# Kernel optimization log

Measured on AMD Instinct MI355X. Metric: run time of the kernel, lower is better.

The kernel has to match this reference:

```python
import jax, jax.numpy as jnp
import numpy as np

EPS = 1e-10
LOSS_COEF = 0.01

def cv_squared(v):
    # torch .var() is unbiased (ddof=1)
    return jnp.var(v, ddof=1) / (jnp.mean(v) ** 2 + EPS)

def setup_inputs() -> dict:
    B, Q, D, H, O, E = 4096, 256, 512, 1024, 512, 16
    key = jax.random.key(0)
    ks = jax.random.split(key, 8)
    return {
        "query": jax.random.normal(ks[0], (B, Q), jnp.float32),
        "x": jax.random.normal(ks[1], (B, D), jnp.float32),
        "w_gate": jax.random.normal(ks[2], (D, E), jnp.float32) * 0.02,
        "task_gate": jax.random.normal(ks[3], (Q, E), jnp.float32) * 0.02,
        "W1": jax.random.normal(ks[4], (E, D, H), jnp.float32) * 0.02,
        "b1": jnp.zeros((E, H), jnp.float32),
        "W2": jax.random.normal(ks[5], (E, H, O), jnp.float32) * 0.02,
        "b2": jnp.zeros((E, O), jnp.float32),
        "k": 4,
    }

def reference(query, x, w_gate, task_gate, W1, b1, W2, b2, k):
    B = x.shape[0]
    E = w_gate.shape[1]
    # --- top-k gating (eval mode: clean logits, no noise) ---
    logits = x @ w_gate + query @ task_gate                      # [B, E]
    m = min(k + 1, E)
    top_vals, top_idx = jax.lax.top_k(logits, m)                 # [B, m]
    topk_gates = jax.nn.softmax(top_vals[:, :k], axis=1)         # [B, k]
    rows = jnp.arange(B)[:, None]
    gates = jnp.zeros_like(logits).at[rows, top_idx[:, :k]].set(topk_gates)  # [B, E]
    importance = gates.sum(0)                                    # [E]
    load = (gates > 0).sum(0).astype(jnp.float32)                # [E]
    loss = LOSS_COEF * (cv_squared(importance) + cv_squared(load))
    # --- dispatch / expert MLP / combine ---
    # gate==0 contributions vanish, so weighting by gates is exactly
    # equivalent to the sparse gather -> expert -> index_add combine.
    y = jnp.zeros((B, W2.shape[2]), jnp.float32)
    for e in range(E):  # fixed small loop over experts
        h = jax.nn.relu(x @ W1[e] + b1[e])                       # [B, H]
        out = h @ W2[e] + b2[e]                                  # [B, O]
        y = y + gates[:, e:e + 1] * out
    return y, loss
```

## Files before the change

kernel.cpp:

```cpp
#include <hip/hip_runtime.h>

typedef short bf16x8_t __attribute__((ext_vector_type(8)));
typedef short bf16x4_t __attribute__((ext_vector_type(4)));
typedef float f32x4_t __attribute__((ext_vector_type(4)));

#define B_DIM 4096
#define Q_DIM 256
#define D_DIM 512
#define H_DIM 1024
#define O_DIM 512
#define E_NUM 16
#define K_TOP 4

#define BM 128
#define BN 128
#define BK 32

__device__ __forceinline__ short f2bf(float f) {
  unsigned int u = __float_as_uint(f);
  u += 0x7FFFu + ((u >> 16) & 1u);
  return (short)(u >> 16);
}

__device__ __forceinline__ void g2l16(const void* g, void* l) {
  __builtin_amdgcn_global_load_lds(
      (const __attribute__((address_space(1))) void*)(unsigned long long)(size_t)g,
      (__attribute__((address_space(3))) void*)(unsigned)(size_t)l, 16, 0, 0);
}

__device__ __forceinline__ void tr_tile(float (*tile)[65], const float* __restrict__ s,
                                        short* __restrict__ d, int R, int C, int r0, int c0,
                                        int t) {
#pragma unroll
  for (int i = 0; i < 16; i++) {
    int lin = i * 256 + t;
    int rr = lin >> 6, cc = lin & 63;
    tile[rr][cc] = s[(size_t)(r0 + rr) * C + (c0 + cc)];
  }
  __syncthreads();
#pragma unroll
  for (int i = 0; i < 2; i++) {
    int task = i * 256 + t;
    int cr = task >> 3, g = task & 7;
    bf16x8_t v;
#pragma unroll
    for (int j = 0; j < 8; j++) v[j] = f2bf(tile[g * 8 + j][cr]);
    *(bf16x8_t*)(d + (size_t)(c0 + cr) * R + r0 + g * 8) = v;
  }
}

__global__ __launch_bounds__(256) void weights_prep(
    const float* __restrict__ W1, const float* __restrict__ W2,
    const float* __restrict__ wg, const float* __restrict__ tg,
    short* __restrict__ w1t, short* __restrict__ w2t, float* __restrict__ wpack) {
  __shared__ float tile[64][65];
  const int blk = blockIdx.x, t = threadIdx.x;
  if (blk < 2048) {
    int e = blk >> 7, rem = blk & 127;
    int r0 = (rem >> 4) * 64, c0 = (rem & 15) * 64;
    tr_tile(tile, W1 + (size_t)e * D_DIM * H_DIM, w1t + (size_t)e * D_DIM * H_DIM,
            D_DIM, H_DIM, r0, c0, t);
  } else if (blk < 4096) {
    int b2 = blk - 2048;
    int e = b2 >> 7, rem = b2 & 127;
    int r0 = (rem >> 3) * 64, c0 = (rem & 7) * 64;
    tr_tile(tile, W2 + (size_t)e * H_DIM * O_DIM, w2t + (size_t)e * H_DIM * O_DIM,
            H_DIM, O_DIM, r0, c0, t);
  } else {
    int lin = (blk - 4096) * 256 + t;
    if (lin < E_NUM * 768) {
      int e = lin / 768, r = lin % 768;
      wpack[lin] = (r < D_DIM) ? wg[r * E_NUM + e] : tg[(r - D_DIM) * E_NUM + e];
    }
  }
}

__global__ __launch_bounds__(256) void gating_kernel(
    const float* __restrict__ x, const float* __restrict__ query,
    const float* __restrict__ wpack,
    int4* __restrict__ topk_e4, float4* __restrict__ topk_g4, short* __restrict__ x_bf) {
  __shared__ __align__(16) float4 s_w[E_NUM * 192];
  const int t = threadIdx.x, wv = t >> 6, lane = t & 63;
  const float4* wp4 = (const float4*)wpack;
#pragma unroll
  for (int i = 0; i < 12; i++) s_w[i * 256 + t] = wp4[i * 256 + t];
  __syncthreads();

  const int row = blockIdx.x * 4 + wv;
  const float4* xr = (const float4*)(x + (size_t)row * D_DIM);
  const float4* qr = (const float4*)(query + (size_t)row * Q_DIM);
  const float4 xv0 = xr[lane], xv1 = xr[64 + lane], qv = qr[lane];

  {
    bf16x4_t v0, v1;
    v0[0] = f2bf(xv0.x); v0[1] = f2bf(xv0.y); v0[2] = f2bf(xv0.z); v0[3] = f2bf(xv0.w);
    v1[0] = f2bf(xv1.x); v1[1] = f2bf(xv1.y); v1[2] = f2bf(xv1.z); v1[3] = f2bf(xv1.w);
    short* xb = x_bf + (size_t)row * D_DIM;
    *(bf16x4_t*)(xb + lane * 4) = v0;
    *(bf16x4_t*)(xb + 256 + lane * 4) = v1;
  }

  float p[E_NUM];
#pragma unroll
  for (int e = 0; e < E_NUM; e++) {
    float4 w0 = s_w[e * 192 + lane];
    float4 w1 = s_w[e * 192 + 64 + lane];
    float4 wq = s_w[e * 192 + 128 + lane];
    p[e] = xv0.x * w0.x + xv0.y * w0.y + xv0.z * w0.z + xv0.w * w0.w +
           xv1.x * w1.x + xv1.y * w1.y + xv1.z * w1.z + xv1.w * w1.w +
           qv.x * wq.x + qv.y * wq.y + qv.z * wq.z + qv.w * wq.w;
  }
#pragma unroll
  for (int e = 0; e < E_NUM; e++) {
    p[e] += __shfl_xor(p[e], 16, 64);
    p[e] += __shfl_xor(p[e], 32, 64);
  }
#pragma unroll
  for (int s = 8; s >= 1; s >>= 1) {
    const bool take = (lane & s) != 0;
#pragma unroll
    for (int j = 0; j < s; j++) {
      float keep = take ? p[j + s] : p[j];
      float send = take ? p[j] : p[j + s];
      p[j] = keep + __shfl_xor(send, s, 64);
    }
  }
  const float logit = p[0];
  float v[E_NUM];
#pragma unroll
  for (int i = 0; i < E_NUM; i++) v[i] = __shfl(logit, i, 64);

  if (lane == 0) {
    int idx[K_TOP];
    float val[K_TOP];
    unsigned used = 0;
    for (int k = 0; k < K_TOP; k++) {
      float best = -3.4e38f;
      int bi = 0;
      for (int i = 0; i < E_NUM; i++)
        if (!(used & (1u << i)) && v[i] > best) { best = v[i]; bi = i; }
      used |= 1u << bi;
      idx[k] = bi;
      val[k] = best;
    }
    float mx = val[0];
    float ex[K_TOP], Z = 0.f;
    for (int k = 0; k < K_TOP; k++) { ex[k] = __expf(val[k] - mx); Z += ex[k]; }
    topk_e4[row] = make_int4(idx[0], idx[1], idx[2], idx[3]);
    topk_g4[row] = make_float4(ex[0] / Z, ex[1] / Z, ex[2] / Z, ex[3] / Z);
  }
}

__global__ __launch_bounds__(256) void csr_kernel(
    const int4* __restrict__ topk_e4, const float4* __restrict__ topk_g4,
    int* __restrict__ count, float* __restrict__ imp_g,
    int* __restrict__ rowlist, int* __restrict__ slotid, float* __restrict__ egate) {
  const int e = blockIdx.x, t = threadIdx.x;
  __shared__ int s_cnt[256];
  __shared__ float s_gs[64];
  int c = 0;
  float gs = 0.f;
#pragma unroll 4
  for (int i = 0; i < 16; i++) {
    int row = t * 16 + i;
    int4 v = topk_e4[row];
    float4 g = topk_g4[row];
    if (v.x == e) { c++; gs += g.x; }
    if (v.y == e) { c++; gs += g.y; }
    if (v.z == e) { c++; gs += g.z; }
    if (v.w == e) { c++; gs += g.w; }
  }
  s_cnt[t] = c;
  float gw = gs;
  for (int off = 32; off >= 1; off >>= 1) gw += __shfl_down(gw, off, 64);
  if ((t & 63) == 0) s_gs[t >> 6] = gw;
  __syncthreads();
  for (int off = 1; off < 256; off <<= 1) {
    int vv = (t >= off) ? s_cnt[t - off] : 0;
    __syncthreads();
    s_cnt[t] += vv;
    __syncthreads();
  }
  int pos = s_cnt[t] - c;
#pragma unroll 4
  for (int i = 0; i < 16; i++) {
    int row = t * 16 + i;
    int4 v = topk_e4[row];
    float4 g = topk_g4[row];
    int ve[4] = {v.x, v.y, v.z, v.w};
    float vg[4] = {g.x, g.y, g.z, g.w};
#pragma unroll
    for (int k = 0; k < K_TOP; k++) {
      if (ve[k] == e) {
        rowlist[e * B_DIM + pos] = row;
        slotid[e * B_DIM + pos] = row * K_TOP + k;
        egate[e * B_DIM + pos] = vg[k];
        pos++;
      }
    }
  }
  if (t == 0) {
    count[e] = s_cnt[255];
    imp_g[e] = s_gs[0] + s_gs[1] + s_gs[2] + s_gs[3];
  }
}

__global__ __launch_bounds__(64) void loss_offsets_kernel(
    const int* __restrict__ count, const float* __restrict__ imp_g,
    int* __restrict__ offs, float* __restrict__ out_loss) {
  if (threadIdx.x == 0) {
    float mi = 0.f, ml = 0.f;
    for (int i = 0; i < E_NUM; i++) { mi += imp_g[i]; ml += (float)count[i]; }
    mi /= (float)E_NUM;
    ml /= (float)E_NUM;
    float vi = 0.f, vl = 0.f;
    for (int i = 0; i < E_NUM; i++) {
      float di = imp_g[i] - mi;
      vi += di * di;
      float dl = (float)count[i] - ml;
      vl += dl * dl;
    }
    vi /= (float)(E_NUM - 1);
    vl /= (float)(E_NUM - 1);
    out_loss[0] = 0.01f * (vi / (mi * mi + 1e-10f) + vl / (ml * ml + 1e-10f));
    int run = 0;
    for (int i = 0; i < E_NUM; i++) { offs[i] = run; run += count[i]; }
  }
}

__global__ __launch_bounds__(256) void gemm1_kernel(
    const short* __restrict__ x_bf, const short* __restrict__ w1t,
    const float* __restrict__ b1, const int* __restrict__ count,
    const int* __restrict__ offs, const int* __restrict__ rowlist,
    short* __restrict__ h_buf) {
  const int flat = blockIdx.x;
  const int xcd = flat & 7, j = flat >> 3;
  const int mt = j & 31, gidx = j >> 5;
  const int group = xcd * 16 + gidx;
  const int e = group >> 3, nt = group & 7;
  const int n_e = count[e];
  if (mt * BM >= n_e) return;
  __shared__ __align__(16) short As[BM * BK];
  __shared__ __align__(16) short Bs[BN * BK];
  const int t = threadIdx.x, lane = t & 63, wv = t >> 6;
  const int wm = wv >> 1, wn = wv & 1;
  const int srow = wv * 16 + (lane >> 2);
  const int kb = (lane & 3) * 8;
  int gr0 = mt * BM + srow;       gr0 = gr0 < n_e ? gr0 : n_e - 1;
  int gr1 = mt * BM + 64 + srow;  gr1 = gr1 < n_e ? gr1 : n_e - 1;
  const short* pa0 = x_bf + (size_t)rowlist[e * B_DIM + gr0] * D_DIM + kb;
  const short* pa1 = x_bf + (size_t)rowlist[e * B_DIM + gr1] * D_DIM + kb;
  const short* w1te = w1t + ((size_t)e * H_DIM + nt * BN) * D_DIM;
  const short* pb0 = w1te + (size_t)srow * D_DIM + kb;
  const short* pb1 = w1te + (size_t)(64 + srow) * D_DIM + kb;
  short* lA0 = As + wv * 16 * BK;
  short* lA1 = As + (64 + wv * 16) * BK;
  short* lB0 = Bs + wv * 16 * BK;
  short* lB1 = Bs + (64 + wv * 16) * BK;

  f32x4_t acc[4][4] = {};
  const int frow = lane & 15, kg = lane >> 4;

  for (int k0 = 0; k0 < D_DIM; k0 += BK) {
    g2l16(pa0 + k0, lA0);
    g2l16(pa1 + k0, lA1);
    g2l16(pb0 + k0, lB0);
    g2l16(pb1 + k0, lB1);
    __syncthreads();
    bf16x8_t af[4], bfr[4];
#pragma unroll
    for (int mi = 0; mi < 4; mi++)
      af[mi] = *(const bf16x8_t*)&As[(wm * 64 + mi * 16 + frow) * BK + kg * 8];
#pragma unroll
    for (int ni = 0; ni < 4; ni++)
      bfr[ni] = *(const bf16x8_t*)&Bs[(wn * 64 + ni * 16 + frow) * BK + kg * 8];
#pragma unroll
    for (int mi = 0; mi < 4; mi++)
#pragma unroll
      for (int ni = 0; ni < 4; ni++)
        acc[mi][ni] = __builtin_amdgcn_mfma_f32_16x16x32_bf16(af[mi], bfr[ni], acc[mi][ni], 0, 0, 0);
    __syncthreads();
  }
  const int obase = offs[e];
#pragma unroll
  for (int mi = 0; mi < 4; mi++) {
#pragma unroll
    for (int r = 0; r < 4; r++) {
      int row = wm * 64 + mi * 16 + kg * 4 + r;
      int m_local = mt * BM + row;
      if (m_local >= n_e) continue;
      size_t hrow = (size_t)(obase + m_local) * H_DIM;
#pragma unroll
      for (int ni = 0; ni < 4; ni++) {
        int col = nt * BN + wn * 64 + ni * 16 + frow;
        float vv = acc[mi][ni][r] + b1[e * H_DIM + col];
        h_buf[hrow + col] = f2bf(vv > 0.f ? vv : 0.f);
      }
    }
  }
}

__global__ __launch_bounds__(256) void gemm2_kernel(
    const short* __restrict__ h_buf, const short* __restrict__ w2t,
    const float* __restrict__ b2, const int* __restrict__ count,
    const int* __restrict__ offs, const int* __restrict__ slotid,
    const float* __restrict__ egate, float* __restrict__ out_buf) {
  const int flat = blockIdx.x;
  const int xcd = flat & 7, j = flat >> 3;
  const int nt = j & 3, gidx = j >> 2;
  const int group = xcd * 64 + gidx;
  const int e = group >> 5, mt = group & 31;
  const int n_e = count[e];
  if (mt * BM >= n_e) return;
  __shared__ __align__(16) short As[BM * BK];
  __shared__ __align__(16) short Bs[BN * BK];
  const int t = threadIdx.x, lane = t & 63, wv = t >> 6;
  const int wm = wv >> 1, wn = wv & 1;
  const int srow = wv * 16 + (lane >> 2);
  const int kb = (lane & 3) * 8;
  const int obase = offs[e];
  int gr0 = mt * BM + srow;       gr0 = gr0 < n_e ? gr0 : n_e - 1;
  int gr1 = mt * BM + 64 + srow;  gr1 = gr1 < n_e ? gr1 : n_e - 1;
  const short* pa0 = h_buf + (size_t)(obase + gr0) * H_DIM + kb;
  const short* pa1 = h_buf + (size_t)(obase + gr1) * H_DIM + kb;
  const short* w2te = w2t + ((size_t)e * O_DIM + nt * BN) * H_DIM;
  const short* pb0 = w2te + (size_t)srow * H_DIM + kb;
  const short* pb1 = w2te + (size_t)(64 + srow) * H_DIM + kb;
  short* lA0 = As + wv * 16 * BK;
  short* lA1 = As + (64 + wv * 16) * BK;
  short* lB0 = Bs + wv * 16 * BK;
  short* lB1 = Bs + (64 + wv * 16) * BK;

  f32x4_t acc[4][4] = {};
  const int frow = lane & 15, kg = lane >> 4;

  for (int k0 = 0; k0 < H_DIM; k0 += BK) {
    g2l16(pa0 + k0, lA0);
    g2l16(pa1 + k0, lA1);
    g2l16(pb0 + k0, lB0);
    g2l16(pb1 + k0, lB1);
    __syncthreads();
    bf16x8_t af[4], bfr[4];
#pragma unroll
    for (int mi = 0; mi < 4; mi++)
      af[mi] = *(const bf16x8_t*)&As[(wm * 64 + mi * 16 + frow) * BK + kg * 8];
#pragma unroll
    for (int ni = 0; ni < 4; ni++)
      bfr[ni] = *(const bf16x8_t*)&Bs[(wn * 64 + ni * 16 + frow) * BK + kg * 8];
#pragma unroll
    for (int mi = 0; mi < 4; mi++)
#pragma unroll
      for (int ni = 0; ni < 4; ni++)
        acc[mi][ni] = __builtin_amdgcn_mfma_f32_16x16x32_bf16(af[mi], bfr[ni], acc[mi][ni], 0, 0, 0);
    __syncthreads();
  }
#pragma unroll
  for (int mi = 0; mi < 4; mi++) {
#pragma unroll
    for (int r = 0; r < 4; r++) {
      int row = wm * 64 + mi * 16 + kg * 4 + r;
      int m_local = mt * BM + row;
      if (m_local >= n_e) continue;
      float g = egate[e * B_DIM + m_local];
      size_t orow = (size_t)slotid[e * B_DIM + m_local] * O_DIM;
#pragma unroll
      for (int ni = 0; ni < 4; ni++) {
        int col = nt * BN + wn * 64 + ni * 16 + frow;
        out_buf[orow + col] = (acc[mi][ni][r] + b2[e * O_DIM + col]) * g;
      }
    }
  }
}

__global__ __launch_bounds__(256) void combine_kernel(const float* __restrict__ out_buf,
                                                      float* __restrict__ y) {
  int idx = blockIdx.x * 256 + threadIdx.x;
  int b = idx >> 7;
  int o = (idx & 127) << 2;
  const float* base = out_buf + (size_t)b * K_TOP * O_DIM + o;
  float4 a0 = *(const float4*)(base);
  float4 a1 = *(const float4*)(base + O_DIM);
  float4 a2 = *(const float4*)(base + 2 * O_DIM);
  float4 a3 = *(const float4*)(base + 3 * O_DIM);
  float4 r;
  r.x = a0.x + a1.x + a2.x + a3.x;
  r.y = a0.y + a1.y + a2.y + a3.y;
  r.z = a0.z + a1.z + a2.z + a3.z;
  r.w = a0.w + a1.w + a2.w + a3.w;
  *(float4*)(y + (size_t)b * O_DIM + o) = r;
}

extern "C" void kernel_launch(void* const* d_in, const int* in_sizes, int n_in,
                              void* d_out, int out_size, void* d_ws, size_t ws_size,
                              hipStream_t stream) {
  (void)in_sizes; (void)n_in; (void)out_size; (void)ws_size;
  const float* query = (const float*)d_in[0];
  const float* x = (const float*)d_in[1];
  const float* wg = (const float*)d_in[2];
  const float* tg = (const float*)d_in[3];
  const float* W1 = (const float*)d_in[4];
  const float* b1 = (const float*)d_in[5];
  const float* W2 = (const float*)d_in[6];
  const float* b2 = (const float*)d_in[7];
  float* y = (float*)d_out;

  char* ws = (char*)d_ws;
  int* count = (int*)(ws + 0);
  float* imp = (float*)(ws + 64);
  int* offs = (int*)(ws + 128);
  int* rowlist = (int*)(ws + 256);
  int* slotid = (int*)(ws + 262400);
  float* egate = (float*)(ws + 524544);
  int4* topk_e4 = (int4*)(ws + 786688);
  float4* topk_g4 = (float4*)(ws + 852224);
  float* wpack = (float*)(ws + 917760);
  short* h_buf = (short*)(ws + 1048576);
  short* w2t = (short*)(ws + 34603008);
  short* x_bf = (short*)(ws + 51380224);
  short* w1t = (short*)(ws + 55574528);
  float* out_buf = (float*)(ws + 51380224);

  weights_prep<<<dim3(4144), 256, 0, stream>>>(W1, W2, wg, tg, w1t, w2t, wpack);
  gating_kernel<<<dim3(B_DIM / 4), 256, 0, stream>>>(x, query, wpack, topk_e4, topk_g4, x_bf);
  csr_kernel<<<dim3(E_NUM), 256, 0, stream>>>(topk_e4, topk_g4, count, imp,
                                              rowlist, slotid, egate);
  loss_offsets_kernel<<<1, 64, 0, stream>>>(count, imp, offs, y + (size_t)B_DIM * O_DIM);
  gemm1_kernel<<<dim3(4096), 256, 0, stream>>>(x_bf, w1t, b1, count, offs, rowlist, h_buf);
  gemm2_kernel<<<dim3(2048), 256, 0, stream>>>(h_buf, w2t, b2, count, offs, slotid, egate,
                                               out_buf);
  combine_kernel<<<dim3(B_DIM * O_DIM / 4 / 256), 256, 0, stream>>>(out_buf, y);
}
```

Baseline: 235.8 us.

## Fuse weight prep with gating and fold loss/offsets into CSR kernel

```diff
diff --git a/kernel.cpp b/kernel.cpp
--- a/kernel.cpp
+++ b/kernel.cpp
@@ -49,44 +49,57 @@
   }
 }
 
-__global__ __launch_bounds__(256) void weights_prep(
+__global__ __launch_bounds__(256) void prep_gate_kernel(
+    const float* __restrict__ x, const float* __restrict__ query,
+    const float* __restrict__ wg, const float* __restrict__ tg,
     const float* __restrict__ W1, const float* __restrict__ W2,
-    const float* __restrict__ wg, const float* __restrict__ tg,
-    short* __restrict__ w1t, short* __restrict__ w2t, float* __restrict__ wpack) {
-  __shared__ float tile[64][65];
+    short* __restrict__ w1t, short* __restrict__ w2t, short* __restrict__ x_bf,
+    int4* __restrict__ topk_e4, float4* __restrict__ topk_g4) {
+  __shared__ __align__(16) float smem[12288];
   const int blk = blockIdx.x, t = threadIdx.x;
-  if (blk < 2048) {
-    int e = blk >> 7, rem = blk & 127;
-    int r0 = (rem >> 4) * 64, c0 = (rem & 15) * 64;
-    tr_tile(tile, W1 + (size_t)e * D_DIM * H_DIM, w1t + (size_t)e * D_DIM * H_DIM,
-            D_DIM, H_DIM, r0, c0, t);
-  } else if (blk < 4096) {
-    int b2 = blk - 2048;
-    int e = b2 >> 7, rem = b2 & 127;
-    int r0 = (rem >> 3) * 64, c0 = (rem & 7) * 64;
-    tr_tile(tile, W2 + (size_t)e * H_DIM * O_DIM, w2t + (size_t)e * H_DIM * O_DIM,
-            H_DIM, O_DIM, r0, c0, t);
-  } else {
-    int lin = (blk - 4096) * 256 + t;
-    if (lin < E_NUM * 768) {
-      int e = lin / 768, r = lin % 768;
-      wpack[lin] = (r < D_DIM) ? wg[r * E_NUM + e] : tg[(r - D_DIM) * E_NUM + e];
-    }
-  }
-}
-
-__global__ __launch_bounds__(256) void gating_kernel(
-    const float* __restrict__ x, const float* __restrict__ query,
-    const float* __restrict__ wpack,
-    int4* __restrict__ topk_e4, float4* __restrict__ topk_g4, short* __restrict__ x_bf) {
-  __shared__ __align__(16) float4 s_w[E_NUM * 192];
-  const int t = threadIdx.x, wv = t >> 6, lane = t & 63;
-  const float4* wp4 = (const float4*)wpack;
-#pragma unroll
-  for (int i = 0; i < 12; i++) s_w[i * 256 + t] = wp4[i * 256 + t];
+
+  if (blk >= 1024) {
+    float(*tile)[65] = (float(*)[65])smem;
+    if (blk < 3072) {
+      int b = blk - 1024;
+      int e = b >> 7, rem = b & 127;
+      int r0 = (rem >> 4) * 64, c0 = (rem & 15) * 64;
+      tr_tile(tile, W1 + (size_t)e * D_DIM * H_DIM, w1t + (size_t)e * D_DIM * H_DIM,
+              D_DIM, H_DIM, r0, c0, t);
+    } else {
+      int b = blk - 3072;
+      int e = b >> 7, rem = b & 127;
+      int r0 = (rem >> 3) * 64, c0 = (rem & 7) * 64;
+      tr_tile(tile, W2 + (size_t)e * H_DIM * O_DIM, w2t + (size_t)e * H_DIM * O_DIM,
+              H_DIM, O_DIM, r0, c0, t);
+    }
+    return;
+  }
+
+#pragma unroll
+  for (int i = 0; i < 12; i++) {
+    int idx4 = (i * 256 + t) * 4;
+    if (idx4 < D_DIM * E_NUM) {
+      float4 v = *(const float4*)(wg + idx4);
+      int d = idx4 >> 4, e0 = idx4 & 15;
+      smem[(e0 + 0) * 768 + d] = v.x;
+      smem[(e0 + 1) * 768 + d] = v.y;
+      smem[(e0 + 2) * 768 + d] = v.z;
+      smem[(e0 + 3) * 768 + d] = v.w;
+    } else {
+      int l2 = idx4 - D_DIM * E_NUM;
+      float4 v = *(const float4*)(tg + l2);
+      int q = l2 >> 4, e0 = l2 & 15;
+      smem[(e0 + 0) * 768 + 512 + q] = v.x;
+      smem[(e0 + 1) * 768 + 512 + q] = v.y;
+      smem[(e0 + 2) * 768 + 512 + q] = v.z;
+      smem[(e0 + 3) * 768 + 512 + q] = v.w;
+    }
+  }
   __syncthreads();
 
-  const int row = blockIdx.x * 4 + wv;
+  const int wv = t >> 6, lane = t & 63;
+  const int row = blk * 4 + wv;
   const float4* xr = (const float4*)(x + (size_t)row * D_DIM);
   const float4* qr = (const float4*)(query + (size_t)row * Q_DIM);
   const float4 xv0 = xr[lane], xv1 = xr[64 + lane], qv = qr[lane];
@@ -100,12 +113,13 @@
     *(bf16x4_t*)(xb + 256 + lane * 4) = v1;
   }
 
+  const float4* s_w4 = (const float4*)smem;
   float p[E_NUM];
 #pragma unroll
   for (int e = 0; e < E_NUM; e++) {
-    float4 w0 = s_w[e * 192 + lane];
-    float4 w1 = s_w[e * 192 + 64 + lane];
-    float4 wq = s_w[e * 192 + 128 + lane];
+    float4 w0 = s_w4[e * 192 + lane];
+    float4 w1 = s_w4[e * 192 + 64 + lane];
+    float4 wq = s_w4[e * 192 + 128 + lane];
     p[e] = xv0.x * w0.x + xv0.y * w0.y + xv0.z * w0.z + xv0.w * w0.w +
            xv1.x * w1.x + xv1.y * w1.y + xv1.z * w1.z + xv1.w * w1.w +
            qv.x * wq.x + qv.y * wq.y + qv.z * wq.z + qv.w * wq.w;
@@ -151,44 +165,56 @@
   }
 }
 
-__global__ __launch_bounds__(256) void csr_kernel(
+__global__ __launch_bounds__(1024) void csr_kernel(
     const int4* __restrict__ topk_e4, const float4* __restrict__ topk_g4,
-    int* __restrict__ count, float* __restrict__ imp_g,
-    int* __restrict__ rowlist, int* __restrict__ slotid, float* __restrict__ egate) {
+    int* __restrict__ count, int* __restrict__ offs,
+    int* __restrict__ rowlist, int* __restrict__ slotid, float* __restrict__ egate,
+    float* __restrict__ out_loss) {
   const int e = blockIdx.x, t = threadIdx.x;
-  __shared__ int s_cnt[256];
-  __shared__ float s_gs[64];
-  int c = 0;
-  float gs = 0.f;
-#pragma unroll 4
-  for (int i = 0; i < 16; i++) {
-    int row = t * 16 + i;
-    int4 v = topk_e4[row];
-    float4 g = topk_g4[row];
-    if (v.x == e) { c++; gs += g.x; }
-    if (v.y == e) { c++; gs += g.y; }
-    if (v.z == e) { c++; gs += g.z; }
-    if (v.w == e) { c++; gs += g.w; }
+  __shared__ int s_cnt[1024];
+  __shared__ int s_lt[16];
+  __shared__ int s_hc[E_NUM];
+  __shared__ float s_hi[E_NUM];
+  if (e == 0 && t < E_NUM) { s_hc[t] = 0; s_hi[t] = 0.f; }
+  __syncthreads();
+
+  int4 v4[4];
+  float4 g4[4];
+  int c = 0, clt = 0;
+#pragma unroll
+  for (int i = 0; i < 4; i++) {
+    int row = t * 4 + i;
+    v4[i] = topk_e4[row];
+    g4[i] = topk_g4[row];
+    int ve[4] = {v4[i].x, v4[i].y, v4[i].z, v4[i].w};
+    float vg[4] = {g4[i].x, g4[i].y, g4[i].z, g4[i].w};
+#pragma unroll
+    for (int k = 0; k < K_TOP; k++) {
+      c += (ve[k] == e);
+      clt += (ve[k] < e);
+      if (e == 0) {
+        atomicAdd(&s_hc[ve[k]], 1);
+        atomicAdd(&s_hi[ve[k]], vg[k]);
+      }
+    }
   }
   s_cnt[t] = c;
-  float gw = gs;
-  for (int off = 32; off >= 1; off >>= 1) gw += __shfl_down(gw, off, 64);
-  if ((t & 63) == 0) s_gs[t >> 6] = gw;
+  int w = clt;
+  for (int off = 32; off >= 1; off >>= 1) w += __shfl_down(w, off, 64);
+  if ((t & 63) == 0) s_lt[t >> 6] = w;
   __syncthreads();
-  for (int off = 1; off < 256; off <<= 1) {
+  for (int off = 1; off < 1024; off <<= 1) {
     int vv = (t >= off) ? s_cnt[t - off] : 0;
     __syncthreads();
     s_cnt[t] += vv;
     __syncthreads();
   }
   int pos = s_cnt[t] - c;
-#pragma unroll 4
-  for (int i = 0; i < 16; i++) {
-    int row = t * 16 + i;
-    int4 v = topk_e4[row];
-    float4 g = topk_g4[row];
-    int ve[4] = {v.x, v.y, v.z, v.w};
-    float vg[4] = {g.x, g.y, g.z, g.w};
+#pragma unroll
+  for (int i = 0; i < 4; i++) {
+    int row = t * 4 + i;
+    int ve[4] = {v4[i].x, v4[i].y, v4[i].z, v4[i].w};
+    float vg[4] = {g4[i].x, g4[i].y, g4[i].z, g4[i].w};
 #pragma unroll
     for (int k = 0; k < K_TOP; k++) {
       if (ve[k] == e) {
@@ -200,31 +226,27 @@
     }
   }
   if (t == 0) {
-    count[e] = s_cnt[255];
-    imp_g[e] = s_gs[0] + s_gs[1] + s_gs[2] + s_gs[3];
-  }
-}
-
-__global__ __launch_bounds__(64) void loss_offsets_kernel(
-    const int* __restrict__ count, const float* __restrict__ imp_g,
-    int* __restrict__ offs, float* __restrict__ out_loss) {
-  if (threadIdx.x == 0) {
+    count[e] = s_cnt[1023];
+    int base = 0;
+    for (int i = 0; i < 16; i++) base += s_lt[i];
+    offs[e] = base;
+  }
+  if (e == 0 && t == 1) {
+    __syncthreads();
     float mi = 0.f, ml = 0.f;
-    for (int i = 0; i < E_NUM; i++) { mi += imp_g[i]; ml += (float)count[i]; }
+    for (int i = 0; i < E_NUM; i++) { mi += s_hi[i]; ml += (float)s_hc[i]; }
     mi /= (float)E_NUM;
     ml /= (float)E_NUM;
     float vi = 0.f, vl = 0.f;
     for (int i = 0; i < E_NUM; i++) {
-      float di = imp_g[i] - mi;
+      float di = s_hi[i] - mi;
       vi += di * di;
-      float dl = (float)count[i] - ml;
+      float dl = (float)s_hc[i] - ml;
       vl += dl * dl;
     }
     vi /= (float)(E_NUM - 1);
     vl /= (float)(E_NUM - 1);
     out_loss[0] = 0.01f * (vi / (mi * mi + 1e-10f) + vl / (ml * ml + 1e-10f));
-    int run = 0;
-    for (int i = 0; i < E_NUM; i++) { offs[i] = run; run += count[i]; }
   }
 }
 
@@ -406,25 +428,23 @@
 
   char* ws = (char*)d_ws;
   int* count = (int*)(ws + 0);
-  float* imp = (float*)(ws + 64);
   int* offs = (int*)(ws + 128);
   int* rowlist = (int*)(ws + 256);
   int* slotid = (int*)(ws + 262400);
   float* egate = (float*)(ws + 524544);
   int4* topk_e4 = (int4*)(ws + 786688);
   float4* topk_g4 = (float4*)(ws + 852224);
-  float* wpack = (float*)(ws + 917760);
   short* h_buf = (short*)(ws + 1048576);
   short* w2t = (short*)(ws + 34603008);
   short* x_bf = (short*)(ws + 51380224);
   short* w1t = (short*)(ws + 55574528);
   float* out_buf = (float*)(ws + 51380224);
 
-  weights_prep<<<dim3(4144), 256, 0, stream>>>(W1, W2, wg, tg, w1t, w2t, wpack);
-  gating_kernel<<<dim3(B_DIM / 4), 256, 0, stream>>>(x, query, wpack, topk_e4, topk_g4, x_bf);
-  csr_kernel<<<dim3(E_NUM), 256, 0, stream>>>(topk_e4, topk_g4, count, imp,
-                                              rowlist, slotid, egate);
-  loss_offsets_kernel<<<1, 64, 0, stream>>>(count, imp, offs, y + (size_t)B_DIM * O_DIM);
+  prep_gate_kernel<<<dim3(5120), 256, 0, stream>>>(x, query, wg, tg, W1, W2,
+                                                   w1t, w2t, x_bf, topk_e4, topk_g4);
+  csr_kernel<<<dim3(E_NUM), 1024, 0, stream>>>(topk_e4, topk_g4, count, offs,
+                                               rowlist, slotid, egate,
+                                               y + (size_t)B_DIM * O_DIM);
   gemm1_kernel<<<dim3(4096), 256, 0, stream>>>(x_bf, w1t, b1, count, offs, rowlist, h_buf);
   gemm2_kernel<<<dim3(2048), 256, 0, stream>>>(h_buf, w2t, b2, count, offs, slotid, egate,
                                                out_buf);
```

Measured after the change: 236.9 us. Within noise of the previous version (+0.5%).
